# Performance work log

Hardware: AMD Instinct MI355X
Metric: run time of the kernel (lower is better)

Reference implementation:

```python
import jax, jax.numpy as jnp
import numpy as np

N_NODES = 50000
N_EDGES = 800000
F_EXP = 128
F_CNV = 64
HID = 128
N_CLASSES = 10
N_GRAPHS = 64
SLOPE = 0.2


def setup_inputs() -> dict:
    key = jax.random.key(0)
    ks = jax.random.split(key, 24)
    inp = {
        "exp": jax.random.normal(ks[0], (N_NODES, F_EXP), dtype=jnp.float32),
        "cnv": jax.random.normal(ks[1], (N_NODES, F_CNV), dtype=jnp.float32),
        "edge_index": jax.random.randint(ks[2], (2, N_EDGES), 0, N_NODES, dtype=jnp.int64 if jax.config.jax_enable_x64 else jnp.int32),
        "batch": jnp.sort(jax.random.randint(ks[3], (N_NODES,), 0, N_GRAPHS)),
    }
    s = 0.02
    def lin(k, fi, fo):
        kw, kb = jax.random.split(k)
        return (jax.random.normal(kw, (fi, fo), jnp.float32) * s,
                jax.random.normal(kb, (fo,), jnp.float32) * s)
    inp["eps1e"] = jnp.zeros((), jnp.float32)
    inp["W1e"], inp["b1e"] = lin(ks[4], F_EXP, HID)
    inp["eps2e"] = jnp.zeros((), jnp.float32)
    inp["W2e"], inp["b2e"] = lin(ks[5], HID, HID)
    inp["eps1c"] = jnp.zeros((), jnp.float32)
    inp["W1c"], inp["b1c"] = lin(ks[6], F_CNV, HID)
    inp["eps2c"] = jnp.zeros((), jnp.float32)
    inp["W2c"], inp["b2c"] = lin(ks[7], HID, HID)
    inp["Wm"], inp["bm"] = lin(ks[8], 2 * HID, HID)
    inp["Wp1"], inp["bp1"] = lin(ks[9], HID, HID)
    inp["Wp2"], inp["bp2"] = lin(ks[10], HID, N_CLASSES)
    return inp


def _lrelu(x):
    return jnp.where(x > 0, x, SLOPE * x)


def _forward(exp, cnv, src, dst, batch,
             eps1e, W1e, b1e, eps2e, W2e, b2e,
             eps1c, W1c, b1c, eps2c, W2c, b2c,
             Wm, bm, Wp1, bp1, Wp2, bp2):
    N = exp.shape[0]

    def gin(x, eps, W, b):
        # scatter-add neighbor aggregation over edges (self-loops included in src/dst)
        agg = jax.ops.segment_sum(x[src], dst, num_segments=N)
        return ((1.0 + eps) * x + agg) @ W + b

    x_exp = _lrelu(gin(exp, eps1e, W1e, b1e))
    x_exp = _lrelu(gin(x_exp, eps2e, W2e, b2e))
    x_cnv = _lrelu(gin(cnv, eps1c, W1c, b1c))
    x_cnv = _lrelu(gin(x_cnv, eps2c, W2c, b2c))
    x = jnp.concatenate([x_exp, x_cnv], axis=1) @ Wm + bm
    x = _lrelu(x)

    # global mean pool over graph ids
    counts = jax.ops.segment_sum(jnp.ones((N,), x.dtype), batch, num_segments=N_GRAPHS)
    counts = jnp.maximum(counts, 1.0)[:, None]
    graph_repr = jax.ops.segment_sum(x, batch, num_segments=N_GRAPHS) / counts

    logits_nodes = _lrelu(x @ Wp1 + bp1)  # nn.ReLU in mlp -> actually ReLU
    logits_nodes = jnp.maximum(x @ Wp1 + bp1, 0.0) @ Wp2 + bp2
    graph_logits = jax.ops.segment_sum(logits_nodes, batch, num_segments=N_GRAPHS) / counts
    return graph_repr, graph_logits


def reference(exp, cnv, edge_index, batch,
              eps1e, W1e, b1e, eps2e, W2e, b2e,
              eps1c, W1c, b1c, eps2c, W2c, b2c,
              Wm, bm, Wp1, bp1, Wp2, bp2):
    N = exp.shape[0]
    loop = jnp.arange(N, dtype=edge_index.dtype)
    src = jnp.concatenate([edge_index[0], loop])
    dst = jnp.concatenate([edge_index[1], loop])
    return _forward(exp, cnv, src, dst, batch,
                    eps1e, W1e, b1e, eps2e, W2e, b2e,
                    eps1c, W1c, b1c, eps2c, W2c, b2c,
                    Wm, bm, Wp1, bp1, Wp2, bp2)
```

## Files before the change

kernel.cpp:

```cpp
#include <hip/hip_runtime.h>

#define N_NODES 50000
#define N_PAD   50016
#define N_EDGES 800000
#define HID 128
#define NCLS 10
#define NG 64
#define PWAVE 32
#define NB_SCAN ((N_NODES + 255) / 256)

#define EPART 8
#define PRANGE ((N_NODES + EPART - 1) / EPART)
#define ECHUNK 4096
#define NCHUNK ((N_EDGES + ECHUNK - 1) / ECHUNK)

typedef unsigned int uint32;
typedef __attribute__((ext_vector_type(8))) short bf16x8;
typedef __attribute__((ext_vector_type(4))) float f32x4;

__device__ __forceinline__ unsigned short f2bf(float f) {
    uint32 u = __float_as_uint(f);
    uint32 r = u + 0x7fffu + ((u >> 16) & 1u);
    return (unsigned short)(r >> 16);
}
__device__ __forceinline__ float bflo(uint32 v) { return __uint_as_float(v << 16); }
__device__ __forceinline__ float bfhi(uint32 v) { return __uint_as_float(v & 0xffff0000u); }
__device__ __forceinline__ uint32 packbf(float a, float b) {
    return (uint32)f2bf(a) | ((uint32)f2bf(b) << 16);
}


__global__ __launch_bounds__(256) void count_part_k(const int* __restrict__ dst,
                                                    int* __restrict__ deg) {
    int part = blockIdx.x & 7;
    int chunk = blockIdx.x >> 3;
    int lo = part * PRANGE;
    int hi = min(lo + PRANGE, N_NODES);
    int e0 = chunk * ECHUNK;
    int e1 = min(e0 + ECHUNK, N_EDGES);
    for (int i = e0 + threadIdx.x; i < e1; i += 256) {
        int d = dst[i];
        if (d >= lo && d < hi) atomicAdd(&deg[d], 1);
    }
}

__global__ __launch_bounds__(256) void scatter_part_k(const int* __restrict__ src,
                                                      const int* __restrict__ dst,
                                                      int* __restrict__ cursor,
                                                      int* __restrict__ csr) {
    int part = blockIdx.x & 7;
    int chunk = blockIdx.x >> 3;
    int lo = part * PRANGE;
    int hi = min(lo + PRANGE, N_NODES);
    int e0 = chunk * ECHUNK;
    int e1 = min(e0 + ECHUNK, N_EDGES);
    for (int i = e0 + threadIdx.x; i < e1; i += 256) {
        int d = dst[i];
        if (d >= lo && d < hi) {
            int pos = atomicAdd(&cursor[d], 1);
            csr[pos] = src[i];
        }
    }
}

__global__ void gbounds_k(const int* __restrict__ batch, int* __restrict__ gstart) {
    int i = blockIdx.x * blockDim.x + threadIdx.x;
    if (i >= N_NODES) return;
    int b = batch[i];
    int prev = (i == 0) ? -1 : batch[i - 1];
    for (int g = prev + 1; g <= b; g++) gstart[g] = i;
    if (i == N_NODES - 1) {
        for (int g = b + 1; g <= NG; g++) gstart[g] = N_NODES;
    }
}

__global__ void gfin_k(const int* __restrict__ gstart, float* __restrict__ invcnt) {
    int g = threadIdx.x;
    if (g < NG) {
        int c = gstart[g + 1] - gstart[g];
        invcnt[g] = (c > 0) ? 1.0f / (float)c : 0.0f;
    }
}

__device__ __forceinline__ int block_excl_scan_256(int v, int tid, int* total_out) {
    int lane = tid & 63, w = tid >> 6;
    int x = v;
#pragma unroll
    for (int off = 1; off < 64; off <<= 1) {
        int y = __shfl_up(x, off, 64);
        if (lane >= off) x += y;
    }
    __shared__ int wsum[4];
    if (lane == 63) wsum[w] = x;
    __syncthreads();
    int add = 0;
#pragma unroll
    for (int i = 0; i < 4; i++) add += (i < w) ? wsum[i] : 0;
    int total = wsum[0] + wsum[1] + wsum[2] + wsum[3];
    if (total_out) *total_out = total;
    return x - v + add;
}

__global__ __launch_bounds__(256) void scan_partial_k(const int* __restrict__ deg,
                                                      int* __restrict__ rowptr,
                                                      int* __restrict__ blocksum) {
    int tid = threadIdx.x;
    int gid = blockIdx.x * 256 + tid;
    int v = (gid < N_NODES) ? deg[gid] : 0;
    int total;
    int excl = block_excl_scan_256(v, tid, &total);
    if (gid < N_NODES) rowptr[gid] = excl;
    if (tid == 0) blocksum[blockIdx.x] = total;
}

__global__ __launch_bounds__(256) void scan_root_k(const int* __restrict__ blocksum,
                                                   int* __restrict__ blockoff) {
    int tid = threadIdx.x;
    int v = (tid < NB_SCAN) ? blocksum[tid] : 0;
    int excl = block_excl_scan_256(v, tid, nullptr);
    if (tid < NB_SCAN) blockoff[tid] = excl;
}

__global__ __launch_bounds__(256) void scan_add_k(int* __restrict__ rowptr,
                                                  int* __restrict__ cursor,
                                                  const int* __restrict__ blockoff) {
    int gid = blockIdx.x * 256 + threadIdx.x;
    if (gid < N_NODES) {
        int r = rowptr[gid] + blockoff[blockIdx.x];
        rowptr[gid] = r;
        cursor[gid] = r;
    }
    if (gid == 0) rowptr[N_NODES] = N_EDGES;
}


__global__ __launch_bounds__(256) void conv_bf_k(const float* __restrict__ in,
                                                 unsigned short* __restrict__ out, int n4) {
    int i = blockIdx.x * 256 + threadIdx.x;
    if (i >= n4) return;
    float4 v = *(const float4*)(in + (size_t)i * 4);
    uint32 lo = packbf(v.x, v.y);
    uint32 hi = packbf(v.z, v.w);
    uint2 o = {lo, hi};
    *(uint2*)(out + (size_t)i * 4) = o;
}

__global__ __launch_bounds__(256) void wconv_all_k(const float* W1e, const float* W2e,
                                                   const float* W1c, const float* W2c,
                                                   const float* Wm, const float* Wp1,
                                                   unsigned short* WT1e, unsigned short* WT2e,
                                                   unsigned short* WT1c, unsigned short* WT2c,
                                                   unsigned short* WTm1, unsigned short* WTm2,
                                                   unsigned short* WTp1) {
    int b = blockIdx.x;
    int t = threadIdx.x;
    const float* W; unsigned short* WT; int i; int K;
    if (b < 64)       { W = W1e; WT = WT1e; i = b * 256 + t;          K = 128; }
    else if (b < 128) { W = W2e; WT = WT2e; i = (b - 64) * 256 + t;   K = 128; }
    else if (b < 160) { W = W1c; WT = WT1c; i = (b - 128) * 256 + t;  K = 64;  }
    else if (b < 224) { W = W2c; WT = WT2c; i = (b - 160) * 256 + t;  K = 128; }
    else if (b < 352) {
        i = (b - 224) * 256 + t;
        int k = i >> 7, n = i & 127;
        unsigned short v = f2bf(Wm[i]);
        if (k < 128) WTm1[n * 128 + k] = v;
        else         WTm2[n * 128 + (k - 128)] = v;
        return;
    }
    else              { W = Wp1; WT = WTp1; i = (b - 352) * 256 + t;  K = 128; }
    int k = i >> 7, n = i & 127;
    if (k < K) WT[n * K + k] = f2bf(W[i]);
}


__global__ __launch_bounds__(256) void agg128_bf_k(const uint32* __restrict__ X,
                                                   const int* __restrict__ rowptr,
                                                   const int* __restrict__ csr,
                                                   const float* __restrict__ eps,
                                                   uint32* __restrict__ H) {
    int wid = (blockIdx.x * 256 + threadIdx.x) >> 6;
    int lane = threadIdx.x & 63;
    if (wid >= N_NODES) return;
    float scale = 2.0f + eps[0];
    uint32 xv = X[(size_t)wid * 64 + lane];
    float a0 = scale * bflo(xv);
    float a1 = scale * bfhi(xv);
    int e = rowptr[wid], e1 = rowptr[wid + 1];
    for (; e + 8 <= e1; e += 8) {
        int i0 = csr[e],     i1 = csr[e + 1], i2 = csr[e + 2], i3 = csr[e + 3];
        int i4 = csr[e + 4], i5 = csr[e + 5], i6 = csr[e + 6], i7 = csr[e + 7];
        uint32 v0 = X[(size_t)i0 * 64 + lane];
        uint32 v1 = X[(size_t)i1 * 64 + lane];
        uint32 v2 = X[(size_t)i2 * 64 + lane];
        uint32 v3 = X[(size_t)i3 * 64 + lane];
        uint32 v4 = X[(size_t)i4 * 64 + lane];
        uint32 v5 = X[(size_t)i5 * 64 + lane];
        uint32 v6 = X[(size_t)i6 * 64 + lane];
        uint32 v7 = X[(size_t)i7 * 64 + lane];
        a0 += bflo(v0) + bflo(v1) + bflo(v2) + bflo(v3) +
              bflo(v4) + bflo(v5) + bflo(v6) + bflo(v7);
        a1 += bfhi(v0) + bfhi(v1) + bfhi(v2) + bfhi(v3) +
              bfhi(v4) + bfhi(v5) + bfhi(v6) + bfhi(v7);
    }
    if (e + 4 <= e1) {
        int i0 = csr[e], i1 = csr[e + 1], i2 = csr[e + 2], i3 = csr[e + 3];
        uint32 v0 = X[(size_t)i0 * 64 + lane];
        uint32 v1 = X[(size_t)i1 * 64 + lane];
        uint32 v2 = X[(size_t)i2 * 64 + lane];
        uint32 v3 = X[(size_t)i3 * 64 + lane];
        a0 += bflo(v0) + bflo(v1) + bflo(v2) + bflo(v3);
        a1 += bfhi(v0) + bfhi(v1) + bfhi(v2) + bfhi(v3);
        e += 4;
    }
    for (; e < e1; e++) {
        uint32 v = X[(size_t)csr[e] * 64 + lane];
        a0 += bflo(v);
        a1 += bfhi(v);
    }
    H[(size_t)wid * 64 + lane] = packbf(a0, a1);
}

__global__ __launch_bounds__(256) void agg64_bf_k(const uint32* __restrict__ X,
                                                  const int* __restrict__ rowptr,
                                                  const int* __restrict__ csr,
                                                  const float* __restrict__ eps,
                                                  uint32* __restrict__ H) {
    int hw = (blockIdx.x * 256 + threadIdx.x) >> 5;
    int lane = threadIdx.x & 31;
    if (hw >= N_NODES) return;
    float scale = 2.0f + eps[0];
    uint32 xv = X[(size_t)hw * 32 + lane];
    float a0 = scale * bflo(xv);
    float a1 = scale * bfhi(xv);
    int e = rowptr[hw], e1 = rowptr[hw + 1];
    for (; e + 8 <= e1; e += 8) {
        int i0 = csr[e],     i1 = csr[e + 1], i2 = csr[e + 2], i3 = csr[e + 3];
        int i4 = csr[e + 4], i5 = csr[e + 5], i6 = csr[e + 6], i7 = csr[e + 7];
        uint32 v0 = X[(size_t)i0 * 32 + lane];
        uint32 v1 = X[(size_t)i1 * 32 + lane];
        uint32 v2 = X[(size_t)i2 * 32 + lane];
        uint32 v3 = X[(size_t)i3 * 32 + lane];
        uint32 v4 = X[(size_t)i4 * 32 + lane];
        uint32 v5 = X[(size_t)i5 * 32 + lane];
        uint32 v6 = X[(size_t)i6 * 32 + lane];
        uint32 v7 = X[(size_t)i7 * 32 + lane];
        a0 += bflo(v0) + bflo(v1) + bflo(v2) + bflo(v3) +
              bflo(v4) + bflo(v5) + bflo(v6) + bflo(v7);
        a1 += bfhi(v0) + bfhi(v1) + bfhi(v2) + bfhi(v3) +
              bfhi(v4) + bfhi(v5) + bfhi(v6) + bfhi(v7);
    }
    if (e + 4 <= e1) {
        int i0 = csr[e], i1 = csr[e + 1], i2 = csr[e + 2], i3 = csr[e + 3];
        uint32 v0 = X[(size_t)i0 * 32 + lane];
        uint32 v1 = X[(size_t)i1 * 32 + lane];
        uint32 v2 = X[(size_t)i2 * 32 + lane];
        uint32 v3 = X[(size_t)i3 * 32 + lane];
        a0 += bflo(v0) + bflo(v1) + bflo(v2) + bflo(v3);
        a1 += bfhi(v0) + bfhi(v1) + bfhi(v2) + bfhi(v3);
        e += 4;
    }
    for (; e < e1; e++) {
        uint32 v = X[(size_t)csr[e] * 32 + lane];
        a0 += bflo(v);
        a1 += bfhi(v);
    }
    H[(size_t)hw * 32 + lane] = packbf(a0, a1);
}


__global__ __launch_bounds__(256) void gemm_bf_k(const unsigned short* __restrict__ A1,
                                                 const unsigned short* __restrict__ WT1, int K1,
                                                 const unsigned short* __restrict__ A2,
                                                 const unsigned short* __restrict__ WT2, int K2,
                                                 const float* __restrict__ bias,
                                                 unsigned short* __restrict__ out, int act) {
    int tid = threadIdx.x;
    int w = tid >> 6, l = tid & 63;
    int row16 = blockIdx.x * 32 + (w & 1) * 16;
    int col16 = (w >> 1) * 64;
    int m = l & 15, g = l >> 4;

    f32x4 acc[4];
#pragma unroll
    for (int nt = 0; nt < 4; nt++) acc[nt] = (f32x4){0.f, 0.f, 0.f, 0.f};

    const unsigned short* A = A1;
    const unsigned short* WT = WT1;
    int K = K1;
    for (int pass = 0; pass < 2; ++pass) {
        if (pass) {
            if (A2 == nullptr) break;
            A = A2; WT = WT2; K = K2;
        }
        const unsigned short* ap = A + (size_t)(row16 + m) * K + g * 8;
        const unsigned short* bp = WT + (size_t)(col16 + m) * K + g * 8;
        for (int k0 = 0; k0 < K; k0 += 32) {
            bf16x8 af = *(const bf16x8*)(ap + k0);
#pragma unroll
            for (int nt = 0; nt < 4; nt++) {
                bf16x8 bfv = *(const bf16x8*)(bp + (size_t)nt * 16 * K + k0);
                acc[nt] = __builtin_amdgcn_mfma_f32_16x16x32_bf16(af, bfv, acc[nt], 0, 0, 0);
            }
        }
    }

#pragma unroll
    for (int nt = 0; nt < 4; nt++) {
        int col = col16 + nt * 16 + m;
        float bv = bias[col];
#pragma unroll
        for (int r = 0; r < 4; r++) {
            int row = row16 + g * 4 + r;
            if (row < N_NODES) {
                float v = acc[nt][r] + bv;
                if (act == 1) v = v > 0.f ? v : 0.2f * v;
                else if (act == 2) v = fmaxf(v, 0.f);
                out[(size_t)row * 128 + col] = f2bf(v);
            }
        }
    }
}


__global__ __launch_bounds__(256) void pool2_bf_k(const uint32* __restrict__ D,
                                                  const uint32* __restrict__ T,
                                                  const int* __restrict__ batch,
                                                  float* __restrict__ sumD,
                                                  float* __restrict__ sumT) {
    int wv = (blockIdx.x * 256 + threadIdx.x) >> 6;
    int f = threadIdx.x & 63;
    int i0 = wv * PWAVE;
    if (i0 >= N_NODES) return;
    int i1 = min(i0 + PWAVE, N_NODES);
    float d0 = 0.f, d1 = 0.f, t0 = 0.f, t1 = 0.f;
    int g = batch[i0];
    int i = i0;
    for (; i + 4 <= i1; i += 4) {
        int b0 = batch[i], b1 = batch[i + 1], b2 = batch[i + 2], b3 = batch[i + 3];
        uint32 dv0 = D[(size_t)i * 64 + f];
        uint32 dv1 = D[(size_t)(i + 1) * 64 + f];
        uint32 dv2 = D[(size_t)(i + 2) * 64 + f];
        uint32 dv3 = D[(size_t)(i + 3) * 64 + f];
        uint32 tv0 = T[(size_t)i * 64 + f];
        uint32 tv1 = T[(size_t)(i + 1) * 64 + f];
        uint32 tv2 = T[(size_t)(i + 2) * 64 + f];
        uint32 tv3 = T[(size_t)(i + 3) * 64 + f];
#define POOL_STEP(bg, dv, tv)                                          \
        if (bg != g) {                                                 \
            atomicAdd(&sumD[g * 128 + 2 * f], d0);                     \
            atomicAdd(&sumD[g * 128 + 2 * f + 1], d1);                 \
            atomicAdd(&sumT[g * 128 + 2 * f], t0);                     \
            atomicAdd(&sumT[g * 128 + 2 * f + 1], t1);                 \
            d0 = d1 = t0 = t1 = 0.f; g = bg;                           \
        }                                                              \
        d0 += bflo(dv); d1 += bfhi(dv);                                \
        t0 += bflo(tv); t1 += bfhi(tv);
        POOL_STEP(b0, dv0, tv0)
        POOL_STEP(b1, dv1, tv1)
        POOL_STEP(b2, dv2, tv2)
        POOL_STEP(b3, dv3, tv3)
    }
    for (; i < i1; i++) {
        int bg = batch[i];
        uint32 dv = D[(size_t)i * 64 + f];
        uint32 tv = T[(size_t)i * 64 + f];
        POOL_STEP(bg, dv, tv)
    }
#undef POOL_STEP
    atomicAdd(&sumD[g * 128 + 2 * f], d0);
    atomicAdd(&sumD[g * 128 + 2 * f + 1], d1);
    atomicAdd(&sumT[g * 128 + 2 * f], t0);
    atomicAdd(&sumT[g * 128 + 2 * f + 1], t1);
}


__global__ __launch_bounds__(128) void finalize_k(const float* __restrict__ sumD,
                                                  const float* __restrict__ sumT,
                                                  const float* __restrict__ invcnt,
                                                  const float* __restrict__ Wp2,
                                                  const float* __restrict__ bp2,
                                                  float* __restrict__ out) {
    __shared__ float tr[128];
    int g = blockIdx.x;
    int f = threadIdx.x;
    float ic = invcnt[g];
    out[g * 128 + f] = sumD[g * 128 + f] * ic;
    tr[f] = sumT[g * 128 + f] * ic;
    __syncthreads();
    if (f < NCLS) {
        float acc = (ic > 0.f) ? bp2[f] : 0.f;
        for (int k = 0; k < 128; k++) acc = fmaf(tr[k], Wp2[k * NCLS + f], acc);
        out[NG * 128 + g * NCLS + f] = acc;
    }
}


extern "C" void kernel_launch(void* const* d_in, const int* in_sizes, int n_in,
                              void* d_out, int out_size, void* d_ws, size_t ws_size,
                              hipStream_t stream) {
    const float* exp_f = (const float*)d_in[0];
    const float* cnv_f = (const float*)d_in[1];
    const int*   ei    = (const int*)d_in[2];
    const int*   batch = (const int*)d_in[3];
    const float* eps1e = (const float*)d_in[4];
    const float* W1e   = (const float*)d_in[5];
    const float* b1e   = (const float*)d_in[6];
    const float* eps2e = (const float*)d_in[7];
    const float* W2e   = (const float*)d_in[8];
    const float* b2e   = (const float*)d_in[9];
    const float* eps1c = (const float*)d_in[10];
    const float* W1c   = (const float*)d_in[11];
    const float* b1c   = (const float*)d_in[12];
    const float* eps2c = (const float*)d_in[13];
    const float* W2c   = (const float*)d_in[14];
    const float* b2c   = (const float*)d_in[15];
    const float* Wm    = (const float*)d_in[16];
    const float* bm    = (const float*)d_in[17];
    const float* Wp1   = (const float*)d_in[18];
    const float* bp1   = (const float*)d_in[19];
    const float* Wp2   = (const float*)d_in[20];
    const float* bp2   = (const float*)d_in[21];
    float* out = (float*)d_out;

    char* ws = (char*)d_ws;
    size_t off = 0;
    auto alloc = [&](size_t bytes) -> void* {
        void* p = ws + off;
        off = (off + bytes + 255) & ~(size_t)255;
        return p;
    };
    int* deg      = (int*)alloc((size_t)N_NODES * 4);
    int* rowptr   = (int*)alloc((size_t)(N_NODES + 1) * 4);
    int* cursor   = (int*)alloc((size_t)N_NODES * 4);
    int* csr      = (int*)alloc((size_t)N_EDGES * 4);
    int* gstart   = (int*)alloc((NG + 1) * 4);
    float* invcnt = (float*)alloc(NG * 4);
    int* blocksum = (int*)alloc(NB_SCAN * 4);
    int* blockoff = (int*)alloc(NB_SCAN * 4);
    float* sumD   = (float*)alloc((size_t)NG * 128 * 4);
    float* sumT   = (float*)alloc((size_t)NG * 128 * 4);

    unsigned short* Xe = (unsigned short*)alloc((size_t)N_PAD * 128 * 2);
    unsigned short* Xc = (unsigned short*)alloc((size_t)N_PAD * 64 * 2);
    unsigned short* E  = (unsigned short*)alloc((size_t)N_PAD * 64 * 2);
    unsigned short* A  = (unsigned short*)alloc((size_t)N_PAD * 128 * 2);
    unsigned short* B  = (unsigned short*)alloc((size_t)N_PAD * 128 * 2);
    unsigned short* C  = (unsigned short*)alloc((size_t)N_PAD * 128 * 2);
    unsigned short* D  = (unsigned short*)alloc((size_t)N_PAD * 128 * 2);
    unsigned short* T  = (unsigned short*)alloc((size_t)N_PAD * 128 * 2);

    unsigned short* WT1e = (unsigned short*)alloc(128 * 128 * 2);
    unsigned short* WT2e = (unsigned short*)alloc(128 * 128 * 2);
    unsigned short* WT1c = (unsigned short*)alloc(128 * 64 * 2);
    unsigned short* WT2c = (unsigned short*)alloc(128 * 128 * 2);
    unsigned short* WTm1 = (unsigned short*)alloc(128 * 128 * 2);
    unsigned short* WTm2 = (unsigned short*)alloc(128 * 128 * 2);
    unsigned short* WTp1 = (unsigned short*)alloc(128 * 128 * 2);

    const int* src = ei;
    const int* dst = ei + N_EDGES;

    hipMemsetAsync(deg, 0, (size_t)N_NODES * 4, stream);
    hipMemsetAsync(sumD, 0, (size_t)NG * 128 * 4 * 2, stream);

    count_part_k<<<NCHUNK * EPART, 256, 0, stream>>>(dst, deg);
    gbounds_k<<<(N_NODES + 255) / 256, 256, 0, stream>>>(batch, gstart);
    scan_partial_k<<<NB_SCAN, 256, 0, stream>>>(deg, rowptr, blocksum);
    scan_root_k<<<1, 256, 0, stream>>>(blocksum, blockoff);
    scan_add_k<<<NB_SCAN, 256, 0, stream>>>(rowptr, cursor, blockoff);
    gfin_k<<<1, 64, 0, stream>>>(gstart, invcnt);
    scatter_part_k<<<NCHUNK * EPART, 256, 0, stream>>>(src, dst, cursor, csr);

    conv_bf_k<<<(N_NODES * 128 / 4 + 255) / 256, 256, 0, stream>>>(exp_f, Xe, N_NODES * 128 / 4);
    conv_bf_k<<<(N_NODES * 64 / 4 + 255) / 256, 256, 0, stream>>>(cnv_f, Xc, N_NODES * 64 / 4);
    wconv_all_k<<<416, 256, 0, stream>>>(W1e, W2e, W1c, W2c, Wm, Wp1,
                                         WT1e, WT2e, WT1c, WT2c, WTm1, WTm2, WTp1);

    const int AGG_GRID = (N_NODES * 64 + 255) / 256;
    const int AGG64_GRID = (N_NODES * 32 + 255) / 256;
    const int GEMM_GRID = (N_NODES + 31) / 32;
    const int POOL_GRID = ((N_NODES + PWAVE - 1) / PWAVE * 64 + 255) / 256;

    agg128_bf_k<<<AGG_GRID, 256, 0, stream>>>((const uint32*)Xe, rowptr, csr, eps1e, (uint32*)A);
    gemm_bf_k<<<GEMM_GRID, 256, 0, stream>>>(A, WT1e, 128, nullptr, nullptr, 0, b1e, B, 1);
    agg128_bf_k<<<AGG_GRID, 256, 0, stream>>>((const uint32*)B, rowptr, csr, eps2e, (uint32*)A);
    gemm_bf_k<<<GEMM_GRID, 256, 0, stream>>>(A, WT2e, 128, nullptr, nullptr, 0, b2e, B, 1);
    agg64_bf_k<<<AGG64_GRID, 256, 0, stream>>>((const uint32*)Xc, rowptr, csr, eps1c, (uint32*)E);
    gemm_bf_k<<<GEMM_GRID, 256, 0, stream>>>(E, WT1c, 64, nullptr, nullptr, 0, b1c, C, 1);
    agg128_bf_k<<<AGG_GRID, 256, 0, stream>>>((const uint32*)C, rowptr, csr, eps2c, (uint32*)A);
    gemm_bf_k<<<GEMM_GRID, 256, 0, stream>>>(A, WT2c, 128, nullptr, nullptr, 0, b2c, C, 1);
    gemm_bf_k<<<GEMM_GRID, 256, 0, stream>>>(B, WTm1, 128, C, WTm2, 128, bm, D, 1);
    gemm_bf_k<<<GEMM_GRID, 256, 0, stream>>>(D, WTp1, 128, nullptr, nullptr, 0, bp1, T, 2);
    pool2_bf_k<<<POOL_GRID, 256, 0, stream>>>((const uint32*)D, (const uint32*)T,
                                              batch, sumD, sumT);
    finalize_k<<<NG, 128, 0, stream>>>(sumD, sumT, invcnt, Wp2, bp2, out);
}
```

Before: 485.1 us.

## Fuse 128-wide aggregation into GEMM and batch both branches' second layer

Adds a kernel that aggregates neighbor rows for 32 nodes into LDS and then runs the bf16 MFMA GEMM with bias and leaky-ReLU directly, removing the intermediate A buffer round trip. The second GIN layers of the exp and cnv branches are launched together in one grid, and the small conversion and invcnt kernels are merged into existing launches. It trades separate, higher-occupancy aggregation waves for a fused block that does gather then compute, which may reduce latency hiding in the gather phase.

```diff
diff --git a/kernel.cpp b/kernel.cpp
--- a/kernel.cpp
+++ b/kernel.cpp
@@ -74,14 +74,6 @@
     }
 }
 
-__global__ void gfin_k(const int* __restrict__ gstart, float* __restrict__ invcnt) {
-    int g = threadIdx.x;
-    if (g < NG) {
-        int c = gstart[g + 1] - gstart[g];
-        invcnt[g] = (c > 0) ? 1.0f / (float)c : 0.0f;
-    }
-}
-
 __device__ __forceinline__ int block_excl_scan_256(int v, int tid, int* total_out) {
     int lane = tid & 63, w = tid >> 6;
     int x = v;
@@ -114,11 +106,17 @@
 }
 
 __global__ __launch_bounds__(256) void scan_root_k(const int* __restrict__ blocksum,
-                                                   int* __restrict__ blockoff) {
+                                                   int* __restrict__ blockoff,
+                                                   const int* __restrict__ gstart,
+                                                   float* __restrict__ invcnt) {
     int tid = threadIdx.x;
     int v = (tid < NB_SCAN) ? blocksum[tid] : 0;
     int excl = block_excl_scan_256(v, tid, nullptr);
     if (tid < NB_SCAN) blockoff[tid] = excl;
+    if (tid < NG) {
+        int c = gstart[tid + 1] - gstart[tid];
+        invcnt[tid] = (c > 0) ? 1.0f / (float)c : 0.0f;
+    }
 }
 
 __global__ __launch_bounds__(256) void scan_add_k(int* __restrict__ rowptr,
@@ -134,14 +132,17 @@
 }
 
 
-__global__ __launch_bounds__(256) void conv_bf_k(const float* __restrict__ in,
-                                                 unsigned short* __restrict__ out, int n4) {
+__global__ __launch_bounds__(256) void conv_both_k(const float* __restrict__ inE,
+                                                   unsigned short* __restrict__ outE, int n4e,
+                                                   const float* __restrict__ inC,
+                                                   unsigned short* __restrict__ outC, int n4c) {
     int i = blockIdx.x * 256 + threadIdx.x;
-    if (i >= n4) return;
+    const float* in;
+    unsigned short* out;
+    if (i < n4e) { in = inE; out = outE; }
+    else { i -= n4e; if (i >= n4c) return; in = inC; out = outC; }
     float4 v = *(const float4*)(in + (size_t)i * 4);
-    uint32 lo = packbf(v.x, v.y);
-    uint32 hi = packbf(v.z, v.w);
-    uint2 o = {lo, hi};
+    uint2 o = {packbf(v.x, v.y), packbf(v.z, v.w)};
     *(uint2*)(out + (size_t)i * 4) = o;
 }
 
@@ -173,19 +174,14 @@
 }
 
 
-__global__ __launch_bounds__(256) void agg128_bf_k(const uint32* __restrict__ X,
-                                                   const int* __restrict__ rowptr,
-                                                   const int* __restrict__ csr,
-                                                   const float* __restrict__ eps,
-                                                   uint32* __restrict__ H) {
-    int wid = (blockIdx.x * 256 + threadIdx.x) >> 6;
-    int lane = threadIdx.x & 63;
-    if (wid >= N_NODES) return;
-    float scale = 2.0f + eps[0];
-    uint32 xv = X[(size_t)wid * 64 + lane];
+__device__ __forceinline__ uint32 agg_row128(const uint32* __restrict__ X,
+                                             const int* __restrict__ rowptr,
+                                             const int* __restrict__ csr,
+                                             int n, int lane, float scale) {
+    uint32 xv = X[(size_t)n * 64 + lane];
     float a0 = scale * bflo(xv);
     float a1 = scale * bfhi(xv);
-    int e = rowptr[wid], e1 = rowptr[wid + 1];
+    int e = rowptr[n], e1 = rowptr[n + 1];
     for (; e + 8 <= e1; e += 8) {
         int i0 = csr[e],     i1 = csr[e + 1], i2 = csr[e + 2], i3 = csr[e + 3];
         int i4 = csr[e + 4], i5 = csr[e + 5], i6 = csr[e + 6], i7 = csr[e + 7];
@@ -217,8 +213,82 @@
         a0 += bflo(v);
         a1 += bfhi(v);
     }
-    H[(size_t)wid * 64 + lane] = packbf(a0, a1);
-}
+    return packbf(a0, a1);
+}
+
+
+__global__ __launch_bounds__(256) void agg_gemm_k(const uint32* __restrict__ X1,
+                                                  const float* __restrict__ eps1,
+                                                  const unsigned short* __restrict__ WT1p,
+                                                  const float* __restrict__ b1,
+                                                  unsigned short* __restrict__ out1,
+                                                  const uint32* __restrict__ X2,
+                                                  const float* __restrict__ eps2,
+                                                  const unsigned short* __restrict__ WT2p,
+                                                  const float* __restrict__ b2,
+                                                  unsigned short* __restrict__ out2,
+                                                  const int* __restrict__ rowptr,
+                                                  const int* __restrict__ csr,
+                                                  int nblk1) {
+    __shared__ uint32 lds[32 * 64];
+    int blk = blockIdx.x;
+    const uint32* X; const float* epsp; const unsigned short* WT;
+    const float* bias; unsigned short* out;
+    if (blk < nblk1) { X = X1; epsp = eps1; WT = WT1p; bias = b1; out = out1; }
+    else { blk -= nblk1; X = X2; epsp = eps2; WT = WT2p; bias = b2; out = out2; }
+
+    int tid = threadIdx.x;
+    int w = tid >> 6, lane = tid & 63;
+    int base = blk * 32;
+    float scale = 2.0f + epsp[0];
+
+    for (int s = 0; s < 8; s++) {
+        int lrow = w * 8 + s;
+        int n = base + lrow;
+        uint32 outv = 0;
+        if (n < N_NODES) outv = agg_row128(X, rowptr, csr, n, lane, scale);
+        int byte = (lrow * 256 + lane * 4) ^ ((lrow & 7) << 4);
+        lds[byte >> 2] = outv;
+    }
+    __syncthreads();
+
+    int m = lane & 15, g = lane >> 4;
+    int lrow = (w & 1) * 16 + m;
+    int row16 = base + (w & 1) * 16;
+    int col16 = (w >> 1) * 64;
+
+    f32x4 acc[4];
+#pragma unroll
+    for (int nt = 0; nt < 4; nt++) acc[nt] = (f32x4){0.f, 0.f, 0.f, 0.f};
+
+    const unsigned short* bp = WT + (size_t)(col16 + m) * 128 + g * 8;
+#pragma unroll
+    for (int k0 = 0; k0 < 128; k0 += 32) {
+        int ab = (lrow * 256 + (g * 8 + k0) * 2) ^ ((lrow & 7) << 4);
+        bf16x8 af = *(const bf16x8*)((const char*)lds + ab);
+#pragma unroll
+        for (int nt = 0; nt < 4; nt++) {
+            bf16x8 bfv = *(const bf16x8*)(bp + (size_t)nt * 16 * 128 + k0);
+            acc[nt] = __builtin_amdgcn_mfma_f32_16x16x32_bf16(af, bfv, acc[nt], 0, 0, 0);
+        }
+    }
+
+#pragma unroll
+    for (int nt = 0; nt < 4; nt++) {
+        int col = col16 + nt * 16 + m;
+        float bv = bias[col];
+#pragma unroll
+        for (int r = 0; r < 4; r++) {
+            int row = row16 + g * 4 + r;
+            if (row < N_NODES) {
+                float v = acc[nt][r] + bv;
+                v = v > 0.f ? v : 0.2f * v;
+                out[(size_t)row * 128 + col] = f2bf(v);
+            }
+        }
+    }
+}
+
 
 __global__ __launch_bounds__(256) void agg64_bf_k(const uint32* __restrict__ X,
                                                   const int* __restrict__ rowptr,
@@ -443,9 +513,10 @@
     unsigned short* Xe = (unsigned short*)alloc((size_t)N_PAD * 128 * 2);
     unsigned short* Xc = (unsigned short*)alloc((size_t)N_PAD * 64 * 2);
     unsigned short* E  = (unsigned short*)alloc((size_t)N_PAD * 64 * 2);
-    unsigned short* A  = (unsigned short*)alloc((size_t)N_PAD * 128 * 2);
     unsigned short* B  = (unsigned short*)alloc((size_t)N_PAD * 128 * 2);
     unsigned short* C  = (unsigned short*)alloc((size_t)N_PAD * 128 * 2);
+    unsigned short* B2 = (unsigned short*)alloc((size_t)N_PAD * 128 * 2);
+    unsigned short* C2 = (unsigned short*)alloc((size_t)N_PAD * 128 * 2);
     unsigned short* D  = (unsigned short*)alloc((size_t)N_PAD * 128 * 2);
     unsigned short* T  = (unsigned short*)alloc((size_t)N_PAD * 128 * 2);
 
@@ -466,31 +537,29 @@
     count_part_k<<<NCHUNK * EPART, 256, 0, stream>>>(dst, deg);
     gbounds_k<<<(N_NODES + 255) / 256, 256, 0, stream>>>(batch, gstart);
     scan_partial_k<<<NB_SCAN, 256, 0, stream>>>(deg, rowptr, blocksum);
-    scan_root_k<<<1, 256, 0, stream>>>(blocksum, blockoff);
+    scan_root_k<<<1, 256, 0, stream>>>(blocksum, blockoff, gstart, invcnt);
     scan_add_k<<<NB_SCAN, 256, 0, stream>>>(rowptr, cursor, blockoff);
-    gfin_k<<<1, 64, 0, stream>>>(gstart, invcnt);
     scatter_part_k<<<NCHUNK * EPART, 256, 0, stream>>>(src, dst, cursor, csr);
 
-    conv_bf_k<<<(N_NODES * 128 / 4 + 255) / 256, 256, 0, stream>>>(exp_f, Xe, N_NODES * 128 / 4);
-    conv_bf_k<<<(N_NODES * 64 / 4 + 255) / 256, 256, 0, stream>>>(cnv_f, Xc, N_NODES * 64 / 4);
+    const int n4e = N_NODES * 128 / 4, n4c = N_NODES * 64 / 4;
+    conv_both_k<<<(n4e + n4c + 255) / 256, 256, 0, stream>>>(exp_f, Xe, n4e, cnv_f, Xc, n4c);
     wconv_all_k<<<416, 256, 0, stream>>>(W1e, W2e, W1c, W2c, Wm, Wp1,
                                          WT1e, WT2e, WT1c, WT2c, WTm1, WTm2, WTp1);
 
-    const int AGG_GRID = (N_NODES * 64 + 255) / 256;
     const int AGG64_GRID = (N_NODES * 32 + 255) / 256;
     const int GEMM_GRID = (N_NODES + 31) / 32;
-    const int POOL_GRID = ((N_NODES + PWAVE - 1) / PWAVE * 64 + 255) / 256;
-
-    agg128_bf_k<<<AGG_GRID, 256, 0, stream>>>((const uint32*)Xe, rowptr, csr, eps1e, (uint32*)A);
-    gemm_bf_k<<<GEMM_GRID, 256, 0, stream>>>(A, WT1e, 128, nullptr, nullptr, 0, b1e, B, 1);
-    agg128_bf_k<<<AGG_GRID, 256, 0, stream>>>((const uint32*)B, rowptr, csr, eps2e, (uint32*)A);
-    gemm_bf_k<<<GEMM_GRID, 256, 0, stream>>>(A, WT2e, 128, nullptr, nullptr, 0, b2e, B, 1);
+
+    agg_gemm_k<<<GEMM_GRID, 256, 0, stream>>>((const uint32*)Xe, eps1e, WT1e, b1e, B,
+                                              nullptr, nullptr, nullptr, nullptr, nullptr,
+                                              rowptr, csr, GEMM_GRID);
     agg64_bf_k<<<AGG64_GRID, 256, 0, stream>>>((const uint32*)Xc, rowptr, csr, eps1c, (uint32*)E);
     gemm_bf_k<<<GEMM_GRID, 256, 0, stream>>>(E, WT1c, 64, nullptr, nullptr, 0, b1c, C, 1);
-    agg128_bf_k<<<AGG_GRID, 256, 0, stream>>>((const uint32*)C, rowptr, csr, eps2c, (uint32*)A);
-    gemm_bf_k<<<GEMM_GRID, 256, 0, stream>>>(A, WT2c, 128, nullptr, nullptr, 0, b2c, C, 1);
-    gemm_bf_k<<<GEMM_GRID, 256, 0, stream>>>(B, WTm1, 128, C, WTm2, 128, bm, D, 1);
+    agg_gemm_k<<<2 * GEMM_GRID, 256, 0, stream>>>((const uint32*)B, eps2e, WT2e, b2e, B2,
+                                                  (const uint32*)C, eps2c, WT2c, b2c, C2,
+                                                  rowptr, csr, GEMM_GRID);
+    gemm_bf_k<<<GEMM_GRID, 256, 0, stream>>>(B2, WTm1, 128, C2, WTm2, 128, bm, D, 1);
     gemm_bf_k<<<GEMM_GRID, 256, 0, stream>>>(D, WTp1, 128, nullptr, nullptr, 0, bp1, T, 2);
+    const int POOL_GRID = ((N_NODES + PWAVE - 1) / PWAVE * 64 + 255) / 256;
     pool2_bf_k<<<POOL_GRID, 256, 0, stream>>>((const uint32*)D, (const uint32*)T,
                                               batch, sumD, sumT);
     finalize_k<<<NG, 128, 0, stream>>>(sumD, sumT, invcnt, Wp2, bp2, out);
```

New measurement: 452.4 us. -6.7%, faster.
